# Optimization experiments

Hardware: AMD Instinct MI355X
Metric: run time of the kernel (lower is better)

Reference implementation:

```python
import jax, jax.numpy as jnp
import numpy as np
import math

B, N, F, H = 16, 256, 1024, 16
HD = F // H  # head_dim = 64
NEG = -9e15


def setup_inputs() -> dict:
    key = jax.random.key(0)
    ks = jax.random.split(key, 12)
    s = 0.02
    return {
        "obj_feats": jax.random.normal(ks[0], (B, N, F), jnp.float32),
        "cross_feats": jax.random.normal(ks[1], (B, N, F), jnp.float32),
        "adj_matrix": jax.random.randint(ks[2], (B, N, N), 0, 2, jnp.int32),
        "label_biases_att": jax.random.normal(ks[3], (B, N, N), jnp.float32),
        "Wq": jax.random.normal(ks[4], (F, F), jnp.float32) * s,
        "bq": jnp.zeros((F,), jnp.float32),
        "Wk": jax.random.normal(ks[5], (F, F), jnp.float32) * s,
        "bk": jnp.zeros((F,), jnp.float32),
        "Wv": jax.random.normal(ks[6], (F, F), jnp.float32) * s,
        "bv": jnp.zeros((F,), jnp.float32),
        # grouped 1x1 conv: out=F, groups=H, in_per_group=F -> weight [F, F]
        "Wo": jax.random.normal(ks[7], (F, F), jnp.float32) * s,
        "bo": jnp.zeros((F,), jnp.float32),
    }


def reference(obj_feats, cross_feats, adj_matrix, label_biases_att,
              Wq, bq, Wk, bk, Wv, bv, Wo, bo):
    # projections (torch Linear: x @ W.T + b)
    q = (jnp.einsum('bnf,gf->bng', obj_feats, Wq) + bq).reshape(B, N, H, HD)
    k = (jnp.einsum('bnf,gf->bng', cross_feats, Wk) + bk).reshape(B, N, H, HD)
    v = jnp.einsum('bnf,gf->bng', cross_feats, Wv) + bv          # [B, N, F] (NOT split per head)

    scale = 1.0 / math.sqrt(float(HD))
    att = jnp.einsum('bqhd,bkhd->bqhk', q, k) * scale            # [B, Nq, H, Nk]

    # adjacency mask broadcast over heads + label bias (both indexed [b, q, k])
    mask = (adj_matrix > 0)[:, :, None, :]                       # [B, Nq, 1, Nk]
    att = jnp.where(mask, att, NEG) + label_biases_att[:, :, None, :]

    p = jax.nn.softmax(att, axis=-1)                             # softmax over keys

    # weighted sum against un-split values: [B, Nq, H, Nk] x [B, Nk, F]
    out = jnp.einsum('bqhk,bkf->bqhf', p, v)                     # [B, Nq, H, F]

    # grouped 1x1 conv: group h maps its F input channels -> HD output channels
    Wo_g = Wo.reshape(H, HD, F)
    out = jnp.einsum('bqhf,hdf->bqhd', out, Wo_g) + bo.reshape(H, HD)
    out = out.reshape(B, N, F)

    att_mean = p.sum(axis=2) / H                                 # [B, Nq, Nk]
    return out, att_mean
```

## Files before the change

kernel.cpp:

```cpp
#include <hip/hip_runtime.h>

#define NEGF -9e15f

typedef __attribute__((ext_vector_type(8))) unsigned short u16x8;
typedef __attribute__((ext_vector_type(8))) short          s16x8;
typedef __attribute__((ext_vector_type(4))) float          f32x4;

__device__ __forceinline__ unsigned short f2bf(float x) {
  union { float f; unsigned int u; } c; c.f = x;
  unsigned int r = c.u + 0x7fffu + ((c.u >> 16) & 1u);
  return (unsigned short)(r >> 16);
}
__device__ __forceinline__ float bf2f(unsigned short v) {
  union { float f; unsigned int u; } c; c.u = ((unsigned int)v) << 16;
  return c.f;
}

__device__ __forceinline__ void gload16(const void* g, void* l) {
  __builtin_amdgcn_global_load_lds(
      (const __attribute__((address_space(1))) unsigned int*)g,
      (__attribute__((address_space(3))) unsigned int*)l, 16, 0, 0);
}

__global__ __launch_bounds__(256) void cvt2_bf16(
    const float* __restrict__ a, const float* __restrict__ b,
    unsigned short* __restrict__ oa, unsigned short* __restrict__ ob)
{
  const int bid = blockIdx.x;
  const float* in = (bid < 4096) ? a : b;
  unsigned short* out = (bid < 4096) ? oa : ob;
  const int i = ((bid & 4095) * 256 + threadIdx.x) * 4;
  const float4 v = *(const float4*)(in + i);
  ushort4 o;
  o.x = f2bf(v.x); o.y = f2bf(v.y); o.z = f2bf(v.z); o.w = f2bf(v.w);
  *(ushort4*)(out + i) = o;
}

__global__ __launch_bounds__(256) void prep_w(
    const float* __restrict__ Wq, const float* __restrict__ Wk,
    const float* __restrict__ Wo, const float* __restrict__ Wv,
    unsigned short* __restrict__ Wall, unsigned short* __restrict__ Wo_bf,
    unsigned short* __restrict__ Wvt_bf)
{
  __shared__ float tile[32][33];
  const int bid = blockIdx.x;
  if (bid < 3072) {
    const int i = ((bid & 1023) * 256 + threadIdx.x) * 4;
    const float* in;
    unsigned short* out;
    float sc = 1.f;
    if (bid < 1024)      { in = Wq; out = Wall;           sc = 0.125f; }
    else if (bid < 2048) { in = Wk; out = Wall + 1048576; }
    else                 { in = Wo; out = Wo_bf; }
    const float4 v = *(const float4*)(in + i);
    ushort4 o;
    o.x = f2bf(v.x * sc); o.y = f2bf(v.y * sc);
    o.z = f2bf(v.z * sc); o.w = f2bf(v.w * sc);
    *(ushort4*)(out + i) = o;
  } else {
    const int j = bid - 3072;
    const int bc = (j & 31) * 32, br = (j >> 5) * 32;
    const int tx = threadIdx.x & 31, ty8 = threadIdx.x >> 5;
    #pragma unroll
    for (int jj = 0; jj < 32; jj += 8)
      tile[ty8 + jj][tx] = Wv[(size_t)(br + ty8 + jj) * 1024 + bc + tx];
    __syncthreads();
    #pragma unroll
    for (int jj = 0; jj < 32; jj += 8)
      Wvt_bf[(size_t)(bc + ty8 + jj) * 1024 + br + tx] = f2bf(tile[tx][ty8 + jj]);
  }
}

__global__ __launch_bounds__(256) void prep_bias(
    const float* __restrict__ bq, const float* __restrict__ bk,
    const float* __restrict__ Wo, const float* __restrict__ bv,
    float* __restrict__ ball)
{
  const int bid = blockIdx.x;
  if (bid < 4) {
    const int i = bid * 256 + threadIdx.x;
    ball[i]        = 0.125f * bq[i];
    ball[1024 + i] = bk[i];
  } else {
    const int g    = (bid - 4) * 4 + (threadIdx.x >> 6);
    const int lane = threadIdx.x & 63;
    float acc = 0.f;
    for (int f = lane; f < 1024; f += 64)
      acc = fmaf(Wo[(size_t)g * 1024 + f], bv[f], acc);
    #pragma unroll
    for (int off = 32; off > 0; off >>= 1) acc += __shfl_down(acc, off);
    if (lane == 0) ball[2048 + g] = acc;
  }
}

__global__ __launch_bounds__(256) void mb_prep(
    const int* __restrict__ adj, const float* __restrict__ lab,
    float* __restrict__ mb)
{
  const int i = (blockIdx.x * 256 + threadIdx.x) * 4;
  const int4   a = *(const int4*)(adj + i);
  const float4 l = *(const float4*)(lab + i);
  float4 o;
  o.x = a.x > 0 ? l.x : NEGF;
  o.y = a.y > 0 ? l.y : NEGF;
  o.z = a.z > 0 ? l.z : NEGF;
  o.w = a.w > 0 ? l.w : NEGF;
  *(float4*)(mb + i) = o;
}

__global__ __launch_bounds__(256) void prep_all(
    const float* __restrict__ obj, const float* __restrict__ cross,
    const float* __restrict__ Wq, const float* __restrict__ Wk,
    const float* __restrict__ Wo, const float* __restrict__ Wv,
    const float* __restrict__ bq, const float* __restrict__ bk,
    const float* __restrict__ bv,
    const int* __restrict__ adj, const float* __restrict__ lab,
    unsigned short* __restrict__ obj_bf, unsigned short* __restrict__ cross_bf,
    unsigned short* __restrict__ Wall, unsigned short* __restrict__ Wo_bf,
    unsigned short* __restrict__ Wvt_bf,
    float* __restrict__ ball, float* __restrict__ mb)
{
  __shared__ float tile[32][33];
  const int bid = blockIdx.x;
  if (bid < 8192) {
    const float* in = (bid < 4096) ? obj : cross;
    unsigned short* out = (bid < 4096) ? obj_bf : cross_bf;
    const int i = ((bid & 4095) * 256 + threadIdx.x) * 4;
    const float4 v = *(const float4*)(in + i);
    ushort4 o;
    o.x = f2bf(v.x); o.y = f2bf(v.y); o.z = f2bf(v.z); o.w = f2bf(v.w);
    *(ushort4*)(out + i) = o;
  } else if (bid < 11264) {
    const int wb = bid - 8192;
    const int i = ((wb & 1023) * 256 + threadIdx.x) * 4;
    const float* in;
    unsigned short* out;
    float sc = 1.f;
    if (wb < 1024)      { in = Wq; out = Wall;           sc = 0.125f; }
    else if (wb < 2048) { in = Wk; out = Wall + 1048576; }
    else                { in = Wo; out = Wo_bf; }
    const float4 v = *(const float4*)(in + i);
    ushort4 o;
    o.x = f2bf(v.x * sc); o.y = f2bf(v.y * sc);
    o.z = f2bf(v.z * sc); o.w = f2bf(v.w * sc);
    *(ushort4*)(out + i) = o;
  } else if (bid < 12288) {
    const int j = bid - 11264;
    const int bc = (j & 31) * 32, br = (j >> 5) * 32;
    const int tx = threadIdx.x & 31, ty8 = threadIdx.x >> 5;
    #pragma unroll
    for (int jj = 0; jj < 32; jj += 8)
      tile[ty8 + jj][tx] = Wv[(size_t)(br + ty8 + jj) * 1024 + bc + tx];
    __syncthreads();
    #pragma unroll
    for (int jj = 0; jj < 32; jj += 8)
      Wvt_bf[(size_t)(bc + ty8 + jj) * 1024 + br + tx] = f2bf(tile[tx][ty8 + jj]);
  } else if (bid < 12548) {
    const int pb = bid - 12288;
    if (pb < 4) {
      const int i = pb * 256 + threadIdx.x;
      ball[i]        = 0.125f * bq[i];
      ball[1024 + i] = bk[i];
    } else {
      const int g    = (pb - 4) * 4 + (threadIdx.x >> 6);
      const int lane = threadIdx.x & 63;
      float acc = 0.f;
      for (int f = lane; f < 1024; f += 64)
        acc = fmaf(Wo[(size_t)g * 1024 + f], bv[f], acc);
      #pragma unroll
      for (int off = 32; off > 0; off >>= 1) acc += __shfl_down(acc, off);
      if (lane == 0) ball[2048 + g] = acc;
    }
  } else {
    const int i = ((bid - 12548) * 256 + threadIdx.x) * 4;
    const int4   a = *(const int4*)(adj + i);
    const float4 l = *(const float4*)(lab + i);
    float4 o;
    o.x = a.x > 0 ? l.x : NEGF;
    o.y = a.y > 0 ? l.y : NEGF;
    o.z = a.z > 0 ? l.z : NEGF;
    o.w = a.w > 0 ? l.w : NEGF;
    *(float4*)(mb + i) = o;
  }
}

__global__ __launch_bounds__(256, 3) void gemm_wov(
    const unsigned short* __restrict__ A,
    const unsigned short* __restrict__ Bw,
    unsigned short* __restrict__ Cout)
{
  __shared__ unsigned short Asm[128 * 64];
  __shared__ unsigned short Bsm[64 * 64];
  const int t = threadIdx.x;
  const int lane = t & 63, w = t >> 6;
  const int wm = w >> 1, wn = w & 1;
  const int bm = blockIdx.y * 128, bn = blockIdx.x * 64;

  const int srow = lane >> 3;
  const int skel = (lane & 7) * 8;
  const int fr = lane & 15, kf = (lane >> 4) * 8;

  f32x4 acc[4][2] = {};

  for (int k0 = 0; k0 < 1024; k0 += 64) {
    if (k0) __syncthreads();
    #pragma unroll
    for (int i = 0; i < 4; ++i) {
      const int c = i * 4 + w;
      const int r = c * 8 + srow;
      gload16(A + (size_t)(bm + r) * 1024 + k0 + skel, &Asm[c * 512]);
    }
    #pragma unroll
    for (int i = 0; i < 2; ++i) {
      const int c = i * 4 + w;
      const int r = c * 8 + srow;
      gload16(Bw + (size_t)(bn + r) * 1024 + k0 + skel, &Bsm[c * 512]);
    }
    __syncthreads();
    #pragma unroll
    for (int kk = 0; kk < 2; ++kk) {
      s16x8 af[4], bf[2];
      #pragma unroll
      for (int fm = 0; fm < 4; ++fm)
        af[fm] = *(const s16x8*)&Asm[(wm * 64 + fm * 16 + fr) * 64 + kk * 32 + kf];
      #pragma unroll
      for (int fn = 0; fn < 2; ++fn)
        bf[fn] = *(const s16x8*)&Bsm[(wn * 32 + fn * 16 + fr) * 64 + kk * 32 + kf];
      #pragma unroll
      for (int fm = 0; fm < 4; ++fm)
        #pragma unroll
        for (int fn = 0; fn < 2; ++fn)
          acc[fm][fn] = __builtin_amdgcn_mfma_f32_16x16x32_bf16(af[fm], bf[fn], acc[fm][fn], 0, 0, 0);
    }
  }

  const int rg = (lane >> 4) * 4;
  #pragma unroll
  for (int fm = 0; fm < 4; ++fm)
    #pragma unroll
    for (int fn = 0; fn < 2; ++fn) {
      const int col = bn + wn * 32 + fn * 16 + fr;
      #pragma unroll
      for (int r = 0; r < 4; ++r) {
        const int row = bm + wm * 64 + fm * 16 + rg + r;
        Cout[(size_t)row * 1024 + col] = f2bf(acc[fm][fn][r]);
      }
    }
}

__global__ __launch_bounds__(512, 2) void gemm_big(
    const unsigned short* __restrict__ objA,
    const unsigned short* __restrict__ crossA,
    const unsigned short* __restrict__ Wall,
    const float* __restrict__ ball,
    unsigned short* __restrict__ Qo,
    unsigned short* __restrict__ Ko,
    unsigned short* __restrict__ VWt)
{
  __shared__ __align__(16) char smem[131072];
  const int t = threadIdx.x;
  const int wid = t >> 6, lane = t & 63;
  const int wm = wid >> 2, wn = wid & 3;
  const int fr = lane & 15, grp = lane >> 4;

  const int bid = blockIdx.x;
  const int xcd = bid & 7, j = bid >> 3;
  const int bmi = (xcd >> 1) * 4 + j / 6;
  const int bni = (xcd & 1) * 6 + j % 6;
  const int bm = bmi * 256, bn = bni * 256;
  const unsigned short* Ag = ((bni < 4) ? objA : crossA) + (size_t)bm * 1024;
  const unsigned short* Bg = Wall + (size_t)bn * 1024;

  const int r8 = lane >> 3, cb = (lane & 7) * 16;

  f32x4 acc[8][4] = {};
  s16x8 bfr[4][2];
  s16x8 aq[2][2];

  auto CH = [&](int buf, int isB, int q, int k0) {
    const int row = q * 64 + wid * 8 + r8;
    const int sc  = cb ^ ((row & 7) << 4);
    const unsigned short* src = isB ? Bg : Ag;
    gload16((const char*)(src + (size_t)row * 1024 + k0) + sc,
            smem + buf * 65536 + isB * 32768 + q * 8192 + wid * 1024);
  };

#define BAR() { asm volatile("" ::: "memory"); __builtin_amdgcn_s_barrier(); asm volatile("" ::: "memory"); }
#define RDB(BUF)                                                             \
  { _Pragma("unroll") for (int fn = 0; fn < 4; ++fn)                         \
      _Pragma("unroll") for (int kk = 0; kk < 2; ++kk) {                     \
        const int row = wn * 64 + fn * 16 + fr;                              \
        bfr[fn][kk] = *(const s16x8*)((BUF) + 32768 + row * 128 +            \
            ((kk * 64 + grp * 16) ^ ((row & 7) << 4)));                      \
      } }
#define RDA(BUF, P)                                                          \
  { _Pragma("unroll") for (int fm = 0; fm < 2; ++fm)                         \
      _Pragma("unroll") for (int kk = 0; kk < 2; ++kk) {                     \
        const int row = wm * 128 + (2 * (P) + fm) * 16 + fr;                 \
        aq[fm][kk] = *(const s16x8*)((BUF) + row * 128 +                     \
            ((kk * 64 + grp * 16) ^ ((row & 7) << 4)));                      \
      } }
#define MMQ(P)                                                               \
  { __builtin_amdgcn_s_setprio(1);                                           \
    _Pragma("unroll") for (int fm = 0; fm < 2; ++fm)                         \
      _Pragma("unroll") for (int fn = 0; fn < 4; ++fn) {                     \
        acc[2 * (P) + fm][fn] = __builtin_amdgcn_mfma_f32_16x16x32_bf16(     \
            aq[fm][0], bfr[fn][0], acc[2 * (P) + fm][fn], 0, 0, 0);          \
        acc[2 * (P) + fm][fn] = __builtin_amdgcn_mfma_f32_16x16x32_bf16(     \
            aq[fm][1], bfr[fn][1], acc[2 * (P) + fm][fn], 0, 0, 0);          \
      }                                                                      \
    __builtin_amdgcn_s_setprio(0); }
#define TILE4(BUF)                                                           \
  RDB(BUF); RDA(BUF, 0); BAR(); MMQ(0); BAR();                               \
  RDA(BUF, 1); BAR(); MMQ(1); BAR();                                         \
  RDA(BUF, 2); BAR(); MMQ(2); BAR();                                         \
  RDA(BUF, 3); BAR(); MMQ(3); BAR();

  CH(0, 1, 0, 0); CH(0, 1, 1, 0); CH(0, 1, 2, 0); CH(0, 1, 3, 0);
  CH(0, 0, 0, 0); CH(0, 0, 1, 0); CH(0, 0, 2, 0); CH(0, 0, 3, 0);
  CH(1, 1, 0, 64); CH(1, 1, 1, 64); CH(1, 1, 2, 64); CH(1, 1, 3, 64);
  CH(1, 0, 0, 64); CH(1, 0, 2, 64);

  #pragma unroll 2
  for (int kt = 0; kt < 14; ++kt) {
    const int cur = kt & 1;
    char* bufc = smem + cur * 65536;
    const int k1 = (kt + 1) * 64, k2 = (kt + 2) * 64;
    CH(cur ^ 1, 0, 1, k1);
    CH(cur ^ 1, 0, 3, k1);
    asm volatile("s_waitcnt vmcnt(8)" ::: "memory");
    BAR();
    RDB(bufc); RDA(bufc, 0);
    BAR(); MMQ(0); BAR();
    RDA(bufc, 1); CH(cur, 1, 0, k2); CH(cur, 1, 1, k2);
    BAR(); MMQ(1); BAR();
    RDA(bufc, 2); CH(cur, 1, 2, k2); CH(cur, 1, 3, k2);
    BAR(); MMQ(2); BAR();
    RDA(bufc, 3); CH(cur, 0, 0, k2); CH(cur, 0, 2, k2);
    BAR(); MMQ(3); BAR();
  }
  CH(1, 0, 1, 960); CH(1, 0, 3, 960);
  asm volatile("s_waitcnt vmcnt(8)" ::: "memory");
  BAR();
  TILE4(smem);
  asm volatile("s_waitcnt vmcnt(0)" ::: "memory");
  BAR();
  TILE4(smem + 65536);

#undef BAR
#undef RDB
#undef RDA
#undef MMQ
#undef TILE4

  const int rg = grp * 4;
  const int mode = bn >> 10;
  #pragma unroll
  for (int fm = 0; fm < 8; ++fm) {
    #pragma unroll
    for (int fn = 0; fn < 4; ++fn) {
      const int col  = bn + wn * 64 + fn * 16 + fr;
      const int cl   = col & 1023;
      const float bb = ball[col];
      const int row0 = bm + wm * 128 + fm * 16 + rg;
      if (mode == 0) {
        #pragma unroll
        for (int r = 0; r < 4; ++r)
          Qo[(size_t)(row0 + r) * 1024 + cl] = f2bf(acc[fm][fn][r] + bb);
      } else if (mode == 1) {
        #pragma unroll
        for (int r = 0; r < 4; ++r)
          Ko[(size_t)(row0 + r) * 1024 + cl] = f2bf(acc[fm][fn][r] + bb);
      } else {
        const int bidx = row0 >> 8, tok = row0 & 255;
        ushort4 u;
        u.x = f2bf(acc[fm][fn][0] + bb);
        u.y = f2bf(acc[fm][fn][1] + bb);
        u.z = f2bf(acc[fm][fn][2] + bb);
        u.w = f2bf(acc[fm][fn][3] + bb);
        *(ushort4*)(VWt + ((size_t)bidx * 1024 + cl) * 256 + tok) = u;
      }
    }
  }
}

__global__ __launch_bounds__(512, 4) void attn_mfma(
    const unsigned short* __restrict__ Qg,
    const unsigned short* __restrict__ Kg,
    const unsigned short* __restrict__ VWt,
    const float* __restrict__ mb,
    const float* __restrict__ bo,
    float* __restrict__ outp, unsigned short* __restrict__ Pb)
{
  const int t = threadIdx.x;
  const int wid = t >> 6, lane = t & 63;
  const int fr = lane & 15, grp = lane >> 4;
  const int bid = blockIdx.x;
  const int xcd = bid & 7, i = bid >> 3;
  const int h    = i & 15;
  const int r2   = i >> 4;
  const int half = r2 & 1;
  const int b    = xcd * 2 + (r2 >> 1);
  const int q0 = half * 128 + wid * 16;

  __shared__ __align__(16) unsigned short Ks[256 * 64];
  __shared__ __align__(16) unsigned short VWs[64 * 256];

  {
    const unsigned short* kb = Kg + (size_t)(b * 256) * 1024 + h * 64;
    const int colb = (lane & 7) * 16;
    #pragma unroll
    for (int c = 0; c < 4; ++c) {
      const int row = c * 64 + wid * 8 + (lane >> 3);
      const int sb  = colb ^ ((row & 7) << 4);
      gload16(kb + (size_t)row * 1024 + (sb >> 1), (char*)Ks + c * 8192 + wid * 1024);
    }
  }
  {
    const unsigned short* vwb = VWt + (size_t)(b * 16 + h) * 16384;
    const int xb = (lane & 31) * 16;
    #pragma unroll
    for (int c = 0; c < 4; ++c) {
      const int row = c * 16 + wid * 2 + (lane >> 5);
      const int sb  = xb ^ ((row & 7) << 4);
      gload16(vwb + row * 256 + (sb >> 1), (char*)VWs + c * 8192 + wid * 1024);
    }
  }

  const unsigned short* qp = Qg + ((size_t)(b * 256 + q0 + fr)) * 1024 + h * 64 + grp * 8;
  const s16x8 qf0 = *(const s16x8*)qp;
  const s16x8 qf1 = *(const s16x8*)(qp + 32);

  __syncthreads();

  const float* mbp = mb + ((size_t)(b * 256 + q0 + fr)) * 256 + grp * 4;
  const int colA = (grp * 16) ^ ((fr & 7) << 4);

  f32x4 s[16];
  #pragma unroll
  for (int nf = 0; nf < 16; ++nf) s[nf] = (f32x4){0.f, 0.f, 0.f, 0.f};

  s16x8 kA[8], kB[8];
  float4 mA[4], mB[4];
  float mx = -3e38f;

#define LOADB(KF, MF, nb)                                                    \
  { _Pragma("unroll") for (int i2 = 0; i2 < 4; ++i2) {                       \
      const char* rp = (const char*)Ks + (((nb)*4 + i2) * 16 + fr) * 128;    \
      KF[2*i2]   = *(const s16x8*)(rp + colA);                               \
      KF[2*i2+1] = *(const s16x8*)(rp + (colA ^ 64));                        \
      MF[i2]     = *(const float4*)(mbp + ((nb)*4 + i2) * 16); } }
#define MFMAB(KF, nb)                                                        \
  { _Pragma("unroll") for (int i2 = 0; i2 < 4; ++i2) {                       \
      s[(nb)*4+i2] = __builtin_amdgcn_mfma_f32_16x16x32_bf16(KF[2*i2],   qf0, s[(nb)*4+i2], 0, 0, 0); \
      s[(nb)*4+i2] = __builtin_amdgcn_mfma_f32_16x16x32_bf16(KF[2*i2+1], qf1, s[(nb)*4+i2], 0, 0, 0); } }
#define MASKB(MF, nb)                                                        \
  { _Pragma("unroll") for (int i2 = 0; i2 < 4; ++i2) {                       \
      _Pragma("unroll") for (int r = 0; r < 4; ++r) {                        \
        const float m = ((const float*)&MF[i2])[r];                          \
        const float v = (m > -1e14f) ? s[(nb)*4+i2][r] + m : m;              \
        s[(nb)*4+i2][r] = v; mx = fmaxf(mx, v); } } }

  LOADB(kA, mA, 0); LOADB(kB, mB, 1); MFMAB(kA, 0);
  MASKB(mA, 0);     LOADB(kA, mA, 2); MFMAB(kB, 1);
  MASKB(mB, 1);     LOADB(kB, mB, 3); MFMAB(kA, 2);
  MASKB(mA, 2);     LOADB(kA, mA, 4); MFMAB(kB, 3);
  MASKB(mB, 3);     LOADB(kB, mB, 5); MFMAB(kA, 4);
  MASKB(mA, 4);     LOADB(kA, mA, 6); MFMAB(kB, 5);
  MASKB(mB, 5);     LOADB(kB, mB, 7); MFMAB(kA, 6);
  MASKB(mA, 6);     MFMAB(kB, 7);     MASKB(mB, 7);
#undef LOADB
#undef MFMAB
#undef MASKB

  mx = fmaxf(mx, __shfl_xor(mx, 16));
  mx = fmaxf(mx, __shfl_xor(mx, 32));
  float sm = 0.f;
  #pragma unroll
  for (int nf = 0; nf < 16; ++nf)
    #pragma unroll
    for (int r = 0; r < 4; ++r) {
      const float e = __expf(s[nf][r] - mx);
      s[nf][r] = e;
      sm += e;
    }
  sm += __shfl_xor(sm, 16);
  sm += __shfl_xor(sm, 32);
  const float inv = 1.f / sm;

  uint2 u2[16];
  #pragma unroll
  for (int nf = 0; nf < 16; ++nf) {
    const unsigned lo = (unsigned)f2bf(s[nf][0] * inv) | ((unsigned)f2bf(s[nf][1] * inv) << 16);
    const unsigned hi = (unsigned)f2bf(s[nf][2] * inv) | ((unsigned)f2bf(s[nf][3] * inv) << 16);
    u2[nf] = make_uint2(lo, hi);
  }

  unsigned short* prow = Pb + (((size_t)(b * 16 + h)) * 256 + q0 + fr) * 256 + grp * 4;
  #pragma unroll
  for (int nf = 0; nf < 16; ++nf)
    *(uint2*)(prow + nf * 16) = u2[nf];

  f32x4 o[4];
  #pragma unroll
  for (int nf = 0; nf < 4; ++nf) o[nf] = (f32x4){0.f, 0.f, 0.f, 0.f};
  const int srcA = fr + ((grp & 1) << 5);
  const int srcB = srcA + 16;
  const int swz  = (fr & 7) << 4;
  const bool hiSel = (grp & 2);
  #pragma unroll
  for (int ks = 0; ks < 8; ++ks) {
    const int aLx = __shfl((int)u2[2 * ks].x,     srcA, 64);
    const int aLy = __shfl((int)u2[2 * ks].y,     srcA, 64);
    const int bLx = __shfl((int)u2[2 * ks].x,     srcB, 64);
    const int bLy = __shfl((int)u2[2 * ks].y,     srcB, 64);
    const int aHx = __shfl((int)u2[2 * ks + 1].x, srcA, 64);
    const int aHy = __shfl((int)u2[2 * ks + 1].y, srcA, 64);
    const int bHx = __shfl((int)u2[2 * ks + 1].x, srcB, 64);
    const int bHy = __shfl((int)u2[2 * ks + 1].y, srcB, 64);
    union { int4 i; s16x8 v; } pf;
    pf.i = hiSel ? make_int4(aHx, aHy, bHx, bHy) : make_int4(aLx, aLy, bLx, bLy);
    const int cbv = (ks * 64 + grp * 16) ^ swz;
    #pragma unroll
    for (int nf = 0; nf < 4; ++nf) {
      const s16x8 vf = *(const s16x8*)((const char*)VWs + (nf * 16 + fr) * 512 + cbv);
      o[nf] = __builtin_amdgcn_mfma_f32_16x16x32_bf16(pf.v, vf, o[nf], 0, 0, 0);
    }
  }

  #pragma unroll
  for (int nf = 0; nf < 4; ++nf) {
    const float bb = bo[h * 64 + nf * 16 + fr];
    #pragma unroll
    for (int r = 0; r < 4; ++r)
      outp[((size_t)b * 256 + q0 + grp * 4 + r) * 1024 + h * 64 + nf * 16 + fr]
          = o[nf][r] + bb;
  }
}

__global__ __launch_bounds__(256) void attm_reduce(
    const unsigned short* __restrict__ Pb, float* __restrict__ attm)
{
  const size_t idx = (size_t)blockIdx.x * 256 + threadIdx.x;
  const int    k8  = (int)(idx & 31);
  const size_t bq  = idx >> 5;
  const int    b   = (int)(bq >> 8);
  const int    q   = (int)(bq & 255);
  float s[8] = {};
  const unsigned short* base = Pb + (size_t)b * 1048576 + (size_t)q * 256 + k8 * 8;
  #pragma unroll
  for (int hh = 0; hh < 16; ++hh) {
    const u16x8 p = *(const u16x8*)(base + (size_t)hh * 65536);
    #pragma unroll
    for (int j = 0; j < 8; ++j) s[j] += bf2f(p[j]);
  }
  float* dst = attm + bq * 256 + k8 * 8;
  float4 r0, r1;
  r0.x = s[0] * 0.0625f; r0.y = s[1] * 0.0625f; r0.z = s[2] * 0.0625f; r0.w = s[3] * 0.0625f;
  r1.x = s[4] * 0.0625f; r1.y = s[5] * 0.0625f; r1.z = s[6] * 0.0625f; r1.w = s[7] * 0.0625f;
  *(float4*)dst = r0;
  *(float4*)(dst + 4) = r1;
}

extern "C" void kernel_launch(void* const* d_in, const int* in_sizes, int n_in,
                              void* d_out, int out_size, void* d_ws, size_t ws_size,
                              hipStream_t stream)
{
  const float* obj   = (const float*)d_in[0];
  const float* cross = (const float*)d_in[1];
  const int*   adj   = (const int*)d_in[2];
  const float* lab   = (const float*)d_in[3];
  const float* Wq    = (const float*)d_in[4];
  const float* bq    = (const float*)d_in[5];
  const float* Wk    = (const float*)d_in[6];
  const float* bk    = (const float*)d_in[7];
  const float* Wv    = (const float*)d_in[8];
  const float* bv    = (const float*)d_in[9];
  const float* Wo    = (const float*)d_in[10];
  const float* bo    = (const float*)d_in[11];

  float* out  = (float*)d_out;
  float* attm = out + (size_t)16 * 256 * 1024;

  char* ws = (char*)d_ws;
  unsigned short* obj_bf   = (unsigned short*)(ws + 0);
  unsigned short* cross_bf = (unsigned short*)(ws + 8388608);
  unsigned short* Qbf      = (unsigned short*)(ws + 16777216);
  unsigned short* Kbf      = (unsigned short*)(ws + 25165824);
  unsigned short* VWt      = (unsigned short*)(ws + 33554432);
  unsigned short* Wall     = (unsigned short*)(ws + 41943040);
  unsigned short* Wo_bf    = (unsigned short*)(ws + 48234496);
  unsigned short* Wvt_bf   = (unsigned short*)(ws + 50331648);
  unsigned short* Pbuf     = (unsigned short*)(ws + 52432896);

  const bool big_ws = ws_size >= (size_t)104857600;

  if (big_ws) {
    float* ball = (float*)(ws + 92274688);
    float* mbuf = (float*)(ws + 96468992);
    prep_all<<<13572, 256, 0, stream>>>(
        obj, cross, Wq, Wk, Wo, Wv, bq, bk, bv, adj, lab,
        obj_bf, cross_bf, Wall, Wo_bf, Wvt_bf, ball, mbuf);
    gemm_wov<<<dim3(16, 8), 256, 0, stream>>>(Wo_bf, Wvt_bf, Wall + 2097152);
    gemm_big<<<192, 512, 0, stream>>>(obj_bf, cross_bf, Wall, ball, Qbf, Kbf, VWt);
    attn_mfma<<<512, 512, 0, stream>>>(Qbf, Kbf, VWt, mbuf, bo, out, Pbuf);
    attm_reduce<<<512, 256, 0, stream>>>(Pbuf, attm);
  } else {
    float* ball = (float*)(ws + 50331648);
    float* mbuf = (float*)obj_bf;
    cvt2_bf16<<<8192, 256, 0, stream>>>(obj, cross, obj_bf, cross_bf);
    prep_w<<<4096, 256, 0, stream>>>(Wq, Wk, Wo, Wv, Wall, Wo_bf, Wvt_bf);
    gemm_wov<<<dim3(16, 8), 256, 0, stream>>>(Wo_bf, Wvt_bf, Wall + 2097152);
    prep_bias<<<260, 256, 0, stream>>>(bq, bk, Wo, bv, ball);
    gemm_big<<<192, 512, 0, stream>>>(obj_bf, cross_bf, Wall, ball, Qbf, Kbf, VWt);
    mb_prep<<<1024, 256, 0, stream>>>(adj, lab, mbuf);
    attn_mfma<<<512, 512, 0, stream>>>(Qbf, Kbf, VWt, mbuf, bo, out, Pbuf);
    attm_reduce<<<512, 256, 0, stream>>>(Pbuf, attm);
  }
}
```

Before: 111.3 us.

## Stage GEMM epilogue through LDS for coalesced stores; retile Wo·Wv GEMM

The large projection GEMM now writes its bf16 results into swizzled shared memory first, then streams them out as 16-byte coalesced rows. This applies both to Q/K and to the transposed V-weights output, replacing the scattered 2-byte and 8-byte global stores. The small Wo·Wv GEMM switches to 64x64 tiles with twice as many blocks to fill more CUs. The attention kernel also issues its first mask-bias loads before the barrier. The cost is an extra barrier and an LDS round trip in the epilogue.

```diff
diff --git a/kernel.cpp b/kernel.cpp
--- a/kernel.cpp
+++ b/kernel.cpp
@@ -189,45 +189,38 @@
     const unsigned short* __restrict__ Bw,
     unsigned short* __restrict__ Cout)
 {
-  __shared__ unsigned short Asm[128 * 64];
+  __shared__ unsigned short Asm[64 * 64];
   __shared__ unsigned short Bsm[64 * 64];
   const int t = threadIdx.x;
   const int lane = t & 63, w = t >> 6;
   const int wm = w >> 1, wn = w & 1;
-  const int bm = blockIdx.y * 128, bn = blockIdx.x * 64;
-
-  const int srow = lane >> 3;
+  const int bm = blockIdx.y * 64, bn = blockIdx.x * 64;
+
   const int skel = (lane & 7) * 8;
   const int fr = lane & 15, kf = (lane >> 4) * 8;
 
-  f32x4 acc[4][2] = {};
+  f32x4 acc[2][2] = {};
 
   for (int k0 = 0; k0 < 1024; k0 += 64) {
     if (k0) __syncthreads();
     #pragma unroll
-    for (int i = 0; i < 4; ++i) {
-      const int c = i * 4 + w;
-      const int r = c * 8 + srow;
-      gload16(A + (size_t)(bm + r) * 1024 + k0 + skel, &Asm[c * 512]);
-    }
-    #pragma unroll
-    for (int i = 0; i < 2; ++i) {
-      const int c = i * 4 + w;
-      const int r = c * 8 + srow;
-      gload16(Bw + (size_t)(bn + r) * 1024 + k0 + skel, &Bsm[c * 512]);
+    for (int c = 0; c < 2; ++c) {
+      const int row = c * 32 + w * 8 + (lane >> 3);
+      gload16(A  + (size_t)(bm + row) * 1024 + k0 + skel, (char*)Asm + c * 4096 + w * 1024);
+      gload16(Bw + (size_t)(bn + row) * 1024 + k0 + skel, (char*)Bsm + c * 4096 + w * 1024);
     }
     __syncthreads();
     #pragma unroll
     for (int kk = 0; kk < 2; ++kk) {
-      s16x8 af[4], bf[2];
+      s16x8 af[2], bf[2];
       #pragma unroll
-      for (int fm = 0; fm < 4; ++fm)
-        af[fm] = *(const s16x8*)&Asm[(wm * 64 + fm * 16 + fr) * 64 + kk * 32 + kf];
+      for (int fm = 0; fm < 2; ++fm)
+        af[fm] = *(const s16x8*)&Asm[(wm * 32 + fm * 16 + fr) * 64 + kk * 32 + kf];
       #pragma unroll
       for (int fn = 0; fn < 2; ++fn)
         bf[fn] = *(const s16x8*)&Bsm[(wn * 32 + fn * 16 + fr) * 64 + kk * 32 + kf];
       #pragma unroll
-      for (int fm = 0; fm < 4; ++fm)
+      for (int fm = 0; fm < 2; ++fm)
         #pragma unroll
         for (int fn = 0; fn < 2; ++fn)
           acc[fm][fn] = __builtin_amdgcn_mfma_f32_16x16x32_bf16(af[fm], bf[fn], acc[fm][fn], 0, 0, 0);
@@ -236,13 +229,13 @@
 
   const int rg = (lane >> 4) * 4;
   #pragma unroll
-  for (int fm = 0; fm < 4; ++fm)
+  for (int fm = 0; fm < 2; ++fm)
     #pragma unroll
     for (int fn = 0; fn < 2; ++fn) {
       const int col = bn + wn * 32 + fn * 16 + fr;
       #pragma unroll
       for (int r = 0; r < 4; ++r) {
-        const int row = bm + wm * 64 + fm * 16 + rg + r;
+        const int row = bm + wm * 32 + fm * 16 + rg + r;
         Cout[(size_t)row * 1024 + col] = f2bf(acc[fm][fn][r]);
       }
     }
@@ -353,33 +346,54 @@
 #undef MMQ
 #undef TILE4
 
+  __syncthreads();
   const int rg = grp * 4;
   const int mode = bn >> 10;
-  #pragma unroll
-  for (int fm = 0; fm < 8; ++fm) {
-    #pragma unroll
-    for (int fn = 0; fn < 4; ++fn) {
-      const int col  = bn + wn * 64 + fn * 16 + fr;
-      const int cl   = col & 1023;
-      const float bb = ball[col];
-      const int row0 = bm + wm * 128 + fm * 16 + rg;
-      if (mode == 0) {
+  if (mode < 2) {
+    #pragma unroll
+    for (int fm = 0; fm < 8; ++fm)
+      #pragma unroll
+      for (int fn = 0; fn < 4; ++fn) {
+        const int col = wn * 64 + fn * 16 + fr;
+        const float bb = ball[bn + col];
+        const int row0 = wm * 128 + fm * 16 + rg;
         #pragma unroll
         for (int r = 0; r < 4; ++r)
-          Qo[(size_t)(row0 + r) * 1024 + cl] = f2bf(acc[fm][fn][r] + bb);
-      } else if (mode == 1) {
-        #pragma unroll
-        for (int r = 0; r < 4; ++r)
-          Ko[(size_t)(row0 + r) * 1024 + cl] = f2bf(acc[fm][fn][r] + bb);
-      } else {
-        const int bidx = row0 >> 8, tok = row0 & 255;
+          *(unsigned short*)(smem + (row0 + r) * 512 +
+              ((col * 2) ^ (((row0 + r) & 7) << 4))) = f2bf(acc[fm][fn][r] + bb);
+      }
+    __syncthreads();
+    unsigned short* dst0 = (mode == 0) ? Qo : Ko;
+    #pragma unroll
+    for (int it = 0; it < 16; ++it) {
+      const int row = it * 16 + wid * 2 + (lane >> 5);
+      const int off = (lane & 31) * 16;
+      *(u16x8*)((char*)(dst0 + (size_t)(bm + row) * 1024 + (bn & 1023)) + off)
+          = *(const u16x8*)(smem + row * 512 + (off ^ ((row & 7) << 4)));
+    }
+  } else {
+    #pragma unroll
+    for (int fm = 0; fm < 8; ++fm)
+      #pragma unroll
+      for (int fn = 0; fn < 4; ++fn) {
+        const int col = wn * 64 + fn * 16 + fr;
+        const float bb = ball[bn + col];
+        const int tok0 = wm * 128 + fm * 16 + rg;
         ushort4 u;
         u.x = f2bf(acc[fm][fn][0] + bb);
         u.y = f2bf(acc[fm][fn][1] + bb);
         u.z = f2bf(acc[fm][fn][2] + bb);
         u.w = f2bf(acc[fm][fn][3] + bb);
-        *(ushort4*)(VWt + ((size_t)bidx * 1024 + cl) * 256 + tok) = u;
+        *(ushort4*)(smem + col * 512 + ((tok0 * 2) ^ ((col & 7) << 4))) = u;
       }
+    __syncthreads();
+    const int bidx = bm >> 8;
+    #pragma unroll
+    for (int it = 0; it < 16; ++it) {
+      const int col = it * 16 + wid * 2 + (lane >> 5);
+      const int off = (lane & 31) * 16;
+      *(u16x8*)((char*)(VWt + ((size_t)bidx * 1024 + (bn & 1023) + col) * 256) + off)
+          = *(const u16x8*)(smem + col * 512 + (off ^ ((col & 7) << 4)));
     }
   }
 }
@@ -430,10 +444,13 @@
   const unsigned short* qp = Qg + ((size_t)(b * 256 + q0 + fr)) * 1024 + h * 64 + grp * 8;
   const s16x8 qf0 = *(const s16x8*)qp;
   const s16x8 qf1 = *(const s16x8*)(qp + 32);
+  const float* mbp = mb + ((size_t)(b * 256 + q0 + fr)) * 256 + grp * 4;
+  float4 mA[4], mB[4];
+  #pragma unroll
+  for (int i2 = 0; i2 < 4; ++i2) mA[i2] = *(const float4*)(mbp + i2 * 16);
 
   __syncthreads();
 
-  const float* mbp = mb + ((size_t)(b * 256 + q0 + fr)) * 256 + grp * 4;
   const int colA = (grp * 16) ^ ((fr & 7) << 4);
 
   f32x4 s[16];
@@ -441,9 +458,13 @@
   for (int nf = 0; nf < 16; ++nf) s[nf] = (f32x4){0.f, 0.f, 0.f, 0.f};
 
   s16x8 kA[8], kB[8];
-  float4 mA[4], mB[4];
   float mx = -3e38f;
 
+#define LOADK(KF, nb)                                                        \
+  { _Pragma("unroll") for (int i2 = 0; i2 < 4; ++i2) {                       \
+      const char* rp = (const char*)Ks + (((nb)*4 + i2) * 16 + fr) * 128;    \
+      KF[2*i2]   = *(const s16x8*)(rp + colA);                               \
+      KF[2*i2+1] = *(const s16x8*)(rp + (colA ^ 64)); } }
 #define LOADB(KF, MF, nb)                                                    \
   { _Pragma("unroll") for (int i2 = 0; i2 < 4; ++i2) {                       \
       const char* rp = (const char*)Ks + (((nb)*4 + i2) * 16 + fr) * 128;    \
@@ -461,7 +482,7 @@
         const float v = (m > -1e14f) ? s[(nb)*4+i2][r] + m : m;              \
         s[(nb)*4+i2][r] = v; mx = fmaxf(mx, v); } } }
 
-  LOADB(kA, mA, 0); LOADB(kB, mB, 1); MFMAB(kA, 0);
+  LOADK(kA, 0);     LOADB(kB, mB, 1); MFMAB(kA, 0);
   MASKB(mA, 0);     LOADB(kA, mA, 2); MFMAB(kB, 1);
   MASKB(mB, 1);     LOADB(kB, mB, 3); MFMAB(kA, 2);
   MASKB(mA, 2);     LOADB(kA, mA, 4); MFMAB(kB, 3);
@@ -469,6 +490,7 @@
   MASKB(mA, 4);     LOADB(kA, mA, 6); MFMAB(kB, 5);
   MASKB(mB, 5);     LOADB(kB, mB, 7); MFMAB(kA, 6);
   MASKB(mA, 6);     MFMAB(kB, 7);     MASKB(mB, 7);
+#undef LOADK
 #undef LOADB
 #undef MFMAB
 #undef MASKB
@@ -601,7 +623,7 @@
     prep_all<<<13572, 256, 0, stream>>>(
         obj, cross, Wq, Wk, Wo, Wv, bq, bk, bv, adj, lab,
         obj_bf, cross_bf, Wall, Wo_bf, Wvt_bf, ball, mbuf);
-    gemm_wov<<<dim3(16, 8), 256, 0, stream>>>(Wo_bf, Wvt_bf, Wall + 2097152);
+    gemm_wov<<<dim3(16, 16), 256, 0, stream>>>(Wo_bf, Wvt_bf, Wall + 2097152);
     gemm_big<<<192, 512, 0, stream>>>(obj_bf, cross_bf, Wall, ball, Qbf, Kbf, VWt);
     attn_mfma<<<512, 512, 0, stream>>>(Qbf, Kbf, VWt, mbuf, bo, out, Pbuf);
     attm_reduce<<<512, 256, 0, stream>>>(Pbuf, attm);
@@ -610,7 +632,7 @@
     float* mbuf = (float*)obj_bf;
     cvt2_bf16<<<8192, 256, 0, stream>>>(obj, cross, obj_bf, cross_bf);
     prep_w<<<4096, 256, 0, stream>>>(Wq, Wk, Wo, Wv, Wall, Wo_bf, Wvt_bf);
-    gemm_wov<<<dim3(16, 8), 256, 0, stream>>>(Wo_bf, Wvt_bf, Wall + 2097152);
+    gemm_wov<<<dim3(16, 16), 256, 0, stream>>>(Wo_bf, Wvt_bf, Wall + 2097152);
     prep_bias<<<260, 256, 0, stream>>>(bq, bk, Wo, bv, ball);
     gemm_big<<<192, 512, 0, stream>>>(obj_bf, cross_bf, Wall, ball, Qbf, Kbf, VWt);
     mb_prep<<<1024, 256, 0, stream>>>(adj, lab, mbuf);
```

Measured after the change: 104.1 us, median of 2. 1.07x faster.
